# Performance work log

Measured on AMD Instinct MI355X. Metric: run time of the kernel, lower is better.

Reference implementation:

```python
import jax, jax.numpy as jnp
import numpy as np

NA, NB = 40000, 40000
D_IN, D_OUT, H, C = 256, 256, 8, 32  # C = D_OUT // H
E = 400000
N_MP = 3


def setup_inputs() -> dict:
    key = jax.random.key(0)
    ks = jax.random.split(key, 16)
    s = 1.0 / np.sqrt(D_IN)
    inp = {
        "x_A": jax.random.normal(ks[0], (NA, D_IN), jnp.float32),
        "x_B": jax.random.normal(ks[1], (NB, D_IN), jnp.float32),
        "edge_ab": jax.random.randint(ks[2], (2, E), 0, NB, jnp.int32),  # src in A, dst in B
        "edge_ba": jax.random.randint(ks[3], (2, E), 0, NA, jnp.int32),  # src in B, dst in A
        "edge_aa": jax.random.randint(ks[4], (2, E), 0, NA, jnp.int32),  # src in A, dst in A
        "W_A": jax.random.normal(ks[5], (D_IN, D_OUT), jnp.float32) * s,
        "b_A": jnp.zeros((D_OUT,), jnp.float32),
        "W_B": jax.random.normal(ks[6], (D_IN, D_OUT), jnp.float32) * s,
        "b_B": jnp.zeros((D_OUT,), jnp.float32),
        "attn_l": jax.random.normal(ks[7], (N_MP, H, C), jnp.float32) * 0.1,
        "attn_r": jax.random.normal(ks[8], (N_MP, H, C), jnp.float32) * 0.1,
        "rel_l_A": jax.random.normal(ks[9], (H, C), jnp.float32) * 0.1,
        "rel_r_A": jax.random.normal(ks[10], (H, C), jnp.float32) * 0.1,
        "rel_l_B": jax.random.normal(ks[11], (H, C), jnp.float32) * 0.1,
        "rel_r_B": jax.random.normal(ks[12], (H, C), jnp.float32) * 0.1,
    }
    return inp


def _leaky(x):
    return jax.nn.leaky_relu(x, negative_slope=0.2)


def _gat_relation(h_src, edge, a_l, a_r, n_dst):
    """GAT-style edge attention + segment softmax + scatter-add.
    h_src: [N_src,H,C], edge: [2,E], a_l: [N_src,H], a_r: [N_dst,H]."""
    src, dst = edge[0], edge[1]
    e = _leaky(a_l[src] + a_r[dst])                      # [E,H]
    m = jax.ops.segment_max(e, dst, num_segments=n_dst)  # [N_dst,H]
    ex = jnp.exp(e - m[dst])
    denom = jax.ops.segment_sum(ex, dst, num_segments=n_dst)
    alpha = ex / denom[dst]                              # softmax over in-neighbors
    msg = h_src[src] * alpha[:, :, None]                 # [E,H,C]
    return jax.ops.segment_sum(msg, dst, num_segments=n_dst)  # [N_dst,H,C]


def _beta_combine(h, rel_embs, rel_l, rel_r):
    """Relation-level attention (get_beta_weights) + weighted sum.
    h: [N,H,C], rel_embs: [N,H,R,C]."""
    bl = (h * rel_l).sum(-1)                                 # [N,H]
    br = (rel_embs * rel_r[None, :, None, :]).sum(-1)        # [N,H,R]
    beta = jax.nn.softmax(_leaky(bl[:, :, None] + br), axis=2)
    out = (rel_embs * beta[..., None]).sum(2)                # [N,H,C]
    return out.reshape(out.shape[0], H * C)


def reference(x_A, x_B, edge_ab, edge_ba, edge_aa, W_A, b_A, W_B, b_B,
              attn_l, attn_r, rel_l_A, rel_r_A, rel_l_B, rel_r_B):
    nA, nB = x_A.shape[0], x_B.shape[0]
    h_A = (x_A @ W_A + b_A).reshape(nA, H, C)
    h_B = (x_B @ W_B + b_B).reshape(nB, H, C)

    # per-metapath node attention scalars (get_alphas)
    # metapath 0: A->B, 1: B->A, 2: A->A
    al0 = (h_A * attn_l[0]).sum(-1); ar0 = (h_B * attn_r[0]).sum(-1)
    al1 = (h_B * attn_l[1]).sum(-1); ar1 = (h_A * attn_r[1]).sum(-1)
    al2 = (h_A * attn_l[2]).sum(-1); ar2 = (h_A * attn_r[2]).sum(-1)

    # aggregate per tail relation (agg_relation_neighbors); last slot = self
    rel_ba = _gat_relation(h_B, edge_ba, al1, ar1, nA)
    rel_aa = _gat_relation(h_A, edge_aa, al2, ar2, nA)
    emb_A = jnp.stack([rel_ba, rel_aa, h_A], axis=2)         # [NA,H,3,C]

    rel_ab = _gat_relation(h_A, edge_ab, al0, ar0, nB)
    emb_B = jnp.stack([rel_ab, h_B], axis=2)                 # [NB,H,2,C]

    out_A = jax.nn.relu(_beta_combine(h_A, emb_A, rel_l_A, rel_r_A))
    out_B = jax.nn.relu(_beta_combine(h_B, emb_B, rel_l_B, rel_r_B))
    return jnp.concatenate([out_A, out_B], axis=0)           # [NA+NB, D_OUT]
```

## Files before the change

### kernel.cpp

```cpp
#include <hip/hip_runtime.h>
#include <math.h>

#define NAn 40000
#define NBn 40000
#define DIN 256
#define DOUT 256
#define NH 8
#define NC 32
#define NE 400000
#define CAP 64

typedef __attribute__((ext_vector_type(8))) short short8;
typedef __attribute__((ext_vector_type(4))) float floatx4;

__device__ __forceinline__ float leaky(float x) { return x > 0.f ? x : 0.2f * x; }
__device__ __forceinline__ float dot4(float4 a, float4 b) {
  return a.x * b.x + a.y * b.y + a.z * b.z + a.w * b.w;
}
__device__ __forceinline__ unsigned bf16_rne_bits(float x) {
  unsigned u = __float_as_uint(x);
  unsigned r = u + 0x7fffu + ((u >> 16) & 1u);
  return r & 0xffff0000u;
}
__device__ __forceinline__ float4 bf4(uint2 u) {
  float4 f;
  f.x = __uint_as_float(u.x << 16);
  f.y = __uint_as_float(u.x & 0xffff0000u);
  f.z = __uint_as_float(u.y << 16);
  f.w = __uint_as_float(u.y & 0xffff0000u);
  return f;
}
__device__ __forceinline__ void bf8(uint4 u, float* f) {
  f[0] = __uint_as_float(u.x << 16);
  f[1] = __uint_as_float(u.x & 0xffff0000u);
  f[2] = __uint_as_float(u.y << 16);
  f[3] = __uint_as_float(u.y & 0xffff0000u);
  f[4] = __uint_as_float(u.z << 16);
  f[5] = __uint_as_float(u.z & 0xffff0000u);
  f[6] = __uint_as_float(u.w << 16);
  f[7] = __uint_as_float(u.w & 0xffff0000u);
}

__global__ void wswz(const float* __restrict__ WA, const float* __restrict__ WB,
                     short8* __restrict__ hiA, short8* __restrict__ loA,
                     short8* __restrict__ hiB, short8* __restrict__ loB) {
  int t = blockIdx.x * blockDim.x + threadIdx.x;
  const float* W;
  short8 *hi, *lo;
  if (t < 8192) {
    W = WA; hi = hiA; lo = loA;
  } else {
    t -= 8192;
    if (t >= 8192) return;
    W = WB; hi = hiB; lo = loB;
  }
  int kt = t >> 10, nt = (t >> 6) & 15, l = t & 63;
  int n = nt * 16 + (l & 15);
  int kb = kt * 32 + (l >> 4) * 8;
  short8 h8, l8;
#pragma unroll
  for (int j = 0; j < 8; ++j) {
    float w = W[(size_t)(kb + j) * DOUT + n];
    unsigned hb = bf16_rne_bits(w);
    h8[j] = (short)(hb >> 16);
    float rem = w - __uint_as_float(hb);
    l8[j] = (short)(bf16_rne_bits(rem) >> 16);
  }
  hi[t] = h8;
  lo[t] = l8;
}

__global__ __launch_bounds__(256) void gemm_mfma(
    const float* __restrict__ XA, const float* __restrict__ XB,
    const short8* __restrict__ WAhi, const short8* __restrict__ WAlo,
    const short8* __restrict__ WBhi, const short8* __restrict__ WBlo,
    const float* __restrict__ bA, const float* __restrict__ bB,
    unsigned* __restrict__ HAbf, unsigned* __restrict__ HBbf) {
  int blk = blockIdx.x;
  const float* X;
  const short8 *Wh, *Wl;
  const float* bias;
  unsigned* Hbf;
  if (blk < NAn / 64) {
    X = XA; Wh = WAhi; Wl = WAlo; bias = bA; Hbf = HAbf;
  } else {
    blk -= NAn / 64;
    X = XB; Wh = WBhi; Wl = WBlo; bias = bB; Hbf = HBbf;
  }
  const int lane = threadIdx.x & 63, wave = threadIdx.x >> 6;
  const int row0 = blk * 64 + wave * 16;
  const int col16 = lane & 15, quad = lane >> 4;
  floatx4 acc[16];
#pragma unroll
  for (int i = 0; i < 16; ++i) acc[i] = (floatx4){0.f, 0.f, 0.f, 0.f};
  const float4* xp = (const float4*)(X + (size_t)(row0 + col16) * DIN + quad * 8);
  for (int kt = 0; kt < 8; ++kt) {
    float4 x0 = xp[kt * 8];
    float4 x1 = xp[kt * 8 + 1];
    float xv[8] = {x0.x, x0.y, x0.z, x0.w, x1.x, x1.y, x1.z, x1.w};
    short8 ahi, alo;
#pragma unroll
    for (int j = 0; j < 8; ++j) {
      unsigned hb = bf16_rne_bits(xv[j]);
      ahi[j] = (short)(hb >> 16);
      float rem = xv[j] - __uint_as_float(hb);
      alo[j] = (short)(bf16_rne_bits(rem) >> 16);
    }
    const short8* bh = Wh + (size_t)kt * 1024 + lane;
    const short8* bl = Wl + (size_t)kt * 1024 + lane;
#pragma unroll
    for (int nt = 0; nt < 16; ++nt) {
      short8 bhv = bh[nt * 64];
      short8 blv = bl[nt * 64];
      acc[nt] = __builtin_amdgcn_mfma_f32_16x16x32_bf16(ahi, bhv, acc[nt], 0, 0, 0);
      acc[nt] = __builtin_amdgcn_mfma_f32_16x16x32_bf16(alo, bhv, acc[nt], 0, 0, 0);
      acc[nt] = __builtin_amdgcn_mfma_f32_16x16x32_bf16(ahi, blv, acc[nt], 0, 0, 0);
    }
  }
#pragma unroll
  for (int nt = 0; nt < 16; ++nt) {
    float bcol = bias[nt * 16 + col16];
#pragma unroll
    for (int r = 0; r < 4; ++r) {
      int row = row0 + quad * 4 + r;
      float v = acc[nt][r] + bcol;
      float vp = __shfl_xor(v, 1);
      if ((lane & 1) == 0) {
        unsigned p = (bf16_rne_bits(v) >> 16) | bf16_rne_bits(vp);
        Hbf[(size_t)row * 128 + nt * 8 + (col16 >> 1)] = p;
      }
    }
  }
}

__global__ void alphas(const uint2* __restrict__ hAbf, const uint2* __restrict__ hBbf,
                       const float* __restrict__ attn_l, const float* __restrict__ attn_r,
                       float* __restrict__ al0, float* __restrict__ ar1,
                       float* __restrict__ al2, float* __restrict__ ar2,
                       float* __restrict__ ar0, float* __restrict__ al1) {
  int idx = blockIdx.x * blockDim.x + threadIdx.x;
  if (idx >= (NAn + NBn) * NH) return;
  bool isA = idx < NAn * NH;
  int k = isA ? idx : idx - NAn * NH;
  int head = k & 7;
  const uint2* h8 = (isA ? hAbf : hBbf) + (size_t)k * 8;
  if (isA) {
    const float4* l0 = (const float4*)(attn_l + 0 * DOUT + head * NC);
    const float4* r1 = (const float4*)(attn_r + 1 * DOUT + head * NC);
    const float4* l2 = (const float4*)(attn_l + 2 * DOUT + head * NC);
    const float4* r2 = (const float4*)(attn_r + 2 * DOUT + head * NC);
    float s0 = 0, s1 = 0, s2 = 0, s3 = 0;
#pragma unroll
    for (int q = 0; q < 8; ++q) {
      float4 hv = bf4(h8[q]);
      s0 += dot4(hv, l0[q]);
      s1 += dot4(hv, r1[q]);
      s2 += dot4(hv, l2[q]);
      s3 += dot4(hv, r2[q]);
    }
    al0[k] = s0;
    ar1[k] = s1;
    al2[k] = s2;
    ar2[k] = s3;
  } else {
    const float4* r0 = (const float4*)(attn_r + 0 * DOUT + head * NC);
    const float4* l1 = (const float4*)(attn_l + 1 * DOUT + head * NC);
    float s0 = 0, s1 = 0;
#pragma unroll
    for (int q = 0; q < 8; ++q) {
      float4 hv = bf4(h8[q]);
      s0 += dot4(hv, r0[q]);
      s1 += dot4(hv, l1[q]);
    }
    ar0[k] = s0;
    al1[k] = s1;
  }
}

__global__ void build_csr3(const int* __restrict__ e_ba, const int* __restrict__ e_aa,
                           const int* __restrict__ e_ab, int* __restrict__ cnt_ba,
                           int* __restrict__ cnt_aa, int* __restrict__ cnt_ab,
                           int* __restrict__ sl_ba, int* __restrict__ sl_aa,
                           int* __restrict__ sl_ab) {
  int i = blockIdx.x * blockDim.x + threadIdx.x;
  if (i >= 3 * NE) return;
  const int* e;
  int* cnt;
  int* sl;
  int k = i;
  if (i < NE) {
    e = e_ba; cnt = cnt_ba; sl = sl_ba;
  } else if (i < 2 * NE) {
    e = e_aa; cnt = cnt_aa; sl = sl_aa; k = i - NE;
  } else {
    e = e_ab; cnt = cnt_ab; sl = sl_ab; k = i - 2 * NE;
  }
  int src = e[k];
  int dst = e[NE + k];
  int pos = atomicAdd(&cnt[dst], 1);
  if (pos < CAP) sl[(size_t)dst * CAP + pos] = src;
}

__device__ __forceinline__ void gat2(int dst, int wave, int lane, int h, int sub, int head,
                                     const int* __restrict__ cnt,
                                     const int* __restrict__ slots,
                                     const float* __restrict__ al,
                                     const float* __restrict__ ar,
                                     const uint4* __restrict__ hbf,
                                     int lds_slot[4][64], float lds_ex[4][512],
                                     float acc[8]) {
#pragma unroll
  for (int k = 0; k < 8; ++k) acc[k] = 0.f;
  int deg = cnt[dst];
  if (deg > CAP) deg = CAP;
  if (deg == 0) return;
  __threadfence_block();
  if (lane < deg) {
    int s = slots[(size_t)dst * CAP + lane];
    lds_slot[wave][lane] = s;
    float4 a0 = *(const float4*)(al + (size_t)s * 8);
    float4 a1 = *(const float4*)(al + (size_t)s * 8 + 4);
    float4 r0 = *(const float4*)(ar + (size_t)dst * 8);
    float4 r1 = *(const float4*)(ar + (size_t)dst * 8 + 4);
    float* exq = &lds_ex[wave][lane * 8];
    exq[0] = __expf(leaky(a0.x + r0.x));
    exq[1] = __expf(leaky(a0.y + r0.y));
    exq[2] = __expf(leaky(a0.z + r0.z));
    exq[3] = __expf(leaky(a0.w + r0.w));
    exq[4] = __expf(leaky(a1.x + r1.x));
    exq[5] = __expf(leaky(a1.y + r1.y));
    exq[6] = __expf(leaky(a1.z + r1.z));
    exq[7] = __expf(leaky(a1.w + r1.w));
  }
  __threadfence_block();
  float den = 0.f;
  int iters = (deg + 1) >> 1;
  for (int it = 0; it < iters; ++it) {
    int j = it * 2 + h;
    if (j < deg) {
      int sj = lds_slot[wave][j];
      float w = lds_ex[wave][j * 8 + head];
      uint4 u = hbf[(size_t)sj * 32 + sub];
      den += w;
      float f[8];
      bf8(u, f);
#pragma unroll
      for (int k = 0; k < 8; ++k) acc[k] += w * f[k];
    }
  }
#pragma unroll
  for (int k = 0; k < 8; ++k) acc[k] += __shfl_xor(acc[k], 32);
  den += __shfl_xor(den, 32);
  float inv = 1.f / den;
#pragma unroll
  for (int k = 0; k < 8; ++k) acc[k] *= inv;
}

__global__ __launch_bounds__(256) void agg_combine(
    const int* __restrict__ cnt_ba, const int* __restrict__ sl_ba,
    const float* __restrict__ al1, const float* __restrict__ ar1,
    const int* __restrict__ cnt_aa, const int* __restrict__ sl_aa,
    const float* __restrict__ al2, const float* __restrict__ ar2,
    const int* __restrict__ cnt_ab, const int* __restrict__ sl_ab,
    const float* __restrict__ al0, const float* __restrict__ ar0,
    const uint4* __restrict__ hAbf, const uint4* __restrict__ hBbf,
    const float* __restrict__ rlA, const float* __restrict__ rrA,
    const float* __restrict__ rlB, const float* __restrict__ rrB,
    float* __restrict__ outp) {
  __shared__ int lds_slot[4][64];
  __shared__ float lds_ex[4][512];
  int wave = threadIdx.x >> 6, lane = threadIdx.x & 63;
  int h = lane >> 5, sub = lane & 31, head = sub >> 2;
  bool isA = blockIdx.x < (NAn / 4);
  int dst = (isA ? blockIdx.x : blockIdx.x - NAn / 4) * 4 + wave;
  float m0[8], hv[8], o[8];
  if (isA) {
    float m1[8];
    gat2(dst, wave, lane, h, sub, head, cnt_ba, sl_ba, al1, ar1, hBbf, lds_slot, lds_ex, m0);
    gat2(dst, wave, lane, h, sub, head, cnt_aa, sl_aa, al2, ar2, hAbf, lds_slot, lds_ex, m1);
    uint4 us = hAbf[(size_t)dst * 32 + sub];
    bf8(us, hv);
    const float4* rl4 = (const float4*)rlA;
    const float4* rr4 = (const float4*)rrA;
    float4 rl0 = rl4[sub * 2], rl1 = rl4[sub * 2 + 1];
    float4 rr0 = rr4[sub * 2], rr1 = rr4[sub * 2 + 1];
    float rl8[8] = {rl0.x, rl0.y, rl0.z, rl0.w, rl1.x, rl1.y, rl1.z, rl1.w};
    float rr8[8] = {rr0.x, rr0.y, rr0.z, rr0.w, rr1.x, rr1.y, rr1.z, rr1.w};
    float pbl = 0, p0 = 0, p1 = 0, p2 = 0;
#pragma unroll
    for (int k = 0; k < 8; ++k) {
      pbl += hv[k] * rl8[k];
      p0 += m0[k] * rr8[k];
      p1 += m1[k] * rr8[k];
      p2 += hv[k] * rr8[k];
    }
#pragma unroll
    for (int d = 1; d < 4; d <<= 1) {
      pbl += __shfl_xor(pbl, d);
      p0 += __shfl_xor(p0, d);
      p1 += __shfl_xor(p1, d);
      p2 += __shfl_xor(p2, d);
    }
    float b0 = leaky(pbl + p0), b1 = leaky(pbl + p1), b2 = leaky(pbl + p2);
    float mx = fmaxf(b0, fmaxf(b1, b2));
    float w0 = __expf(b0 - mx), w1 = __expf(b1 - mx), w2 = __expf(b2 - mx);
    float inv = 1.f / (w0 + w1 + w2);
    w0 *= inv; w1 *= inv; w2 *= inv;
#pragma unroll
    for (int k = 0; k < 8; ++k)
      o[k] = fmaxf(0.f, m0[k] * w0 + m1[k] * w1 + hv[k] * w2);
  } else {
    gat2(dst, wave, lane, h, sub, head, cnt_ab, sl_ab, al0, ar0, hAbf, lds_slot, lds_ex, m0);
    uint4 us = hBbf[(size_t)dst * 32 + sub];
    bf8(us, hv);
    const float4* rl4 = (const float4*)rlB;
    const float4* rr4 = (const float4*)rrB;
    float4 rl0 = rl4[sub * 2], rl1 = rl4[sub * 2 + 1];
    float4 rr0 = rr4[sub * 2], rr1 = rr4[sub * 2 + 1];
    float rl8[8] = {rl0.x, rl0.y, rl0.z, rl0.w, rl1.x, rl1.y, rl1.z, rl1.w};
    float rr8[8] = {rr0.x, rr0.y, rr0.z, rr0.w, rr1.x, rr1.y, rr1.z, rr1.w};
    float pbl = 0, p0 = 0, p1 = 0;
#pragma unroll
    for (int k = 0; k < 8; ++k) {
      pbl += hv[k] * rl8[k];
      p0 += m0[k] * rr8[k];
      p1 += hv[k] * rr8[k];
    }
#pragma unroll
    for (int d = 1; d < 4; d <<= 1) {
      pbl += __shfl_xor(pbl, d);
      p0 += __shfl_xor(p0, d);
      p1 += __shfl_xor(p1, d);
    }
    float b0 = leaky(pbl + p0), b1 = leaky(pbl + p1);
    float mx = fmaxf(b0, b1);
    float w0 = __expf(b0 - mx), w1 = __expf(b1 - mx);
    float inv = 1.f / (w0 + w1);
    w0 *= inv; w1 *= inv;
#pragma unroll
    for (int k = 0; k < 8; ++k) o[k] = fmaxf(0.f, m0[k] * w0 + hv[k] * w1);
  }
  float* orow = outp + (size_t)(isA ? dst : NAn + dst) * DOUT + sub * 8;
  if (h == 0) {
    *(float4*)orow = (float4){o[0], o[1], o[2], o[3]};
    *(float4*)(orow + 4) = (float4){o[4], o[5], o[6], o[7]};
  }
}

extern "C" void kernel_launch(void* const* d_in, const int* in_sizes, int n_in, void* d_out,
                              int out_size, void* d_ws, size_t ws_size, hipStream_t stream) {
  const float* xA = (const float*)d_in[0];
  const float* xB = (const float*)d_in[1];
  const int* e_ab = (const int*)d_in[2];
  const int* e_ba = (const int*)d_in[3];
  const int* e_aa = (const int*)d_in[4];
  const float* WA = (const float*)d_in[5];
  const float* bA = (const float*)d_in[6];
  const float* WB = (const float*)d_in[7];
  const float* bB = (const float*)d_in[8];
  const float* attn_l = (const float*)d_in[9];
  const float* attn_r = (const float*)d_in[10];
  const float* rlA = (const float*)d_in[11];
  const float* rrA = (const float*)d_in[12];
  const float* rlB = (const float*)d_in[13];
  const float* rrB = (const float*)d_in[14];
  float* out = (float*)d_out;

  char* p = (char*)d_ws;
  auto alloc = [&](size_t bytes) -> char* {
    char* r = p;
    p += (bytes + 255) & ~(size_t)255;
    return r;
  };
  unsigned* hAbf = (unsigned*)alloc((size_t)NAn * DOUT * 2);
  unsigned* hBbf = (unsigned*)alloc((size_t)NBn * DOUT * 2);
  float* al0 = (float*)alloc((size_t)NAn * NH * 4);
  float* ar1 = (float*)alloc((size_t)NAn * NH * 4);
  float* al2 = (float*)alloc((size_t)NAn * NH * 4);
  float* ar2 = (float*)alloc((size_t)NAn * NH * 4);
  float* ar0 = (float*)alloc((size_t)NBn * NH * 4);
  float* al1 = (float*)alloc((size_t)NBn * NH * 4);
  short8* WAhi = (short8*)alloc((size_t)8192 * 16);
  short8* WAlo = (short8*)alloc((size_t)8192 * 16);
  short8* WBhi = (short8*)alloc((size_t)8192 * 16);
  short8* WBlo = (short8*)alloc((size_t)8192 * 16);
  int* cnts = (int*)alloc((size_t)3 * NAn * 4);
  int* cnt_ba = cnts;
  int* cnt_aa = cnts + NAn;
  int* cnt_ab = cnts + 2 * NAn;
  int* slots_ba = (int*)alloc((size_t)NAn * CAP * 4);
  int* slots_aa = (int*)alloc((size_t)NAn * CAP * 4);
  int* slots_ab = (int*)alloc((size_t)NBn * CAP * 4);

  hipMemsetAsync(cnts, 0, (size_t)3 * NAn * 4, stream);

  wswz<<<64, 256, 0, stream>>>(WA, WB, WAhi, WAlo, WBhi, WBlo);
  build_csr3<<<(3 * NE + 255) / 256, 256, 0, stream>>>(e_ba, e_aa, e_ab, cnt_ba, cnt_aa,
                                                       cnt_ab, slots_ba, slots_aa, slots_ab);
  gemm_mfma<<<(NAn + NBn) / 64, 256, 0, stream>>>(xA, xB, WAhi, WAlo, WBhi, WBlo, bA, bB,
                                                  hAbf, hBbf);
  alphas<<<((NAn + NBn) * NH + 255) / 256, 256, 0, stream>>>(
      (const uint2*)hAbf, (const uint2*)hBbf, attn_l, attn_r, al0, ar1, al2, ar2, ar0, al1);
  agg_combine<<<(NAn + NBn) / 4, 256, 0, stream>>>(
      cnt_ba, slots_ba, al1, ar1, cnt_aa, slots_aa, al2, ar2, cnt_ab, slots_ab, al0, ar0,
      (const uint4*)hAbf, (const uint4*)hBbf, rlA, rrA, rlB, rrB, out);
}
```

Baseline: 476.5 us.

## Drop weight low-part split and stage weight fragments in double-buffered LDS

The GEMM stops splitting the weight matrix into hi/lo bf16 parts, so each tile needs two MFMAs instead of three and the low-weight buffer and its swizzle output go away. Weight fragments are now loaded cooperatively into a double-buffered shared-memory tile, with the next k-slice prefetched into registers while the current one is computed. Each wave no longer fetches all weight fragments from global memory on its own. This lowers GEMM precision, since the weight low-order residual is dropped, and adds a block barrier per k-step.

```diff
diff --git a/kernel.cpp b/kernel.cpp
--- a/kernel.cpp
+++ b/kernel.cpp
@@ -42,59 +42,74 @@
 }
 
 __global__ void wswz(const float* __restrict__ WA, const float* __restrict__ WB,
-                     short8* __restrict__ hiA, short8* __restrict__ loA,
-                     short8* __restrict__ hiB, short8* __restrict__ loB) {
+                     short8* __restrict__ hiA, short8* __restrict__ hiB) {
   int t = blockIdx.x * blockDim.x + threadIdx.x;
   const float* W;
-  short8 *hi, *lo;
+  short8* hi;
   if (t < 8192) {
-    W = WA; hi = hiA; lo = loA;
+    W = WA; hi = hiA;
   } else {
     t -= 8192;
     if (t >= 8192) return;
-    W = WB; hi = hiB; lo = loB;
+    W = WB; hi = hiB;
   }
   int kt = t >> 10, nt = (t >> 6) & 15, l = t & 63;
   int n = nt * 16 + (l & 15);
   int kb = kt * 32 + (l >> 4) * 8;
-  short8 h8, l8;
+  short8 h8;
 #pragma unroll
   for (int j = 0; j < 8; ++j) {
     float w = W[(size_t)(kb + j) * DOUT + n];
-    unsigned hb = bf16_rne_bits(w);
-    h8[j] = (short)(hb >> 16);
-    float rem = w - __uint_as_float(hb);
-    l8[j] = (short)(bf16_rne_bits(rem) >> 16);
+    h8[j] = (short)(bf16_rne_bits(w) >> 16);
   }
   hi[t] = h8;
-  lo[t] = l8;
 }
 
 __global__ __launch_bounds__(256) void gemm_mfma(
     const float* __restrict__ XA, const float* __restrict__ XB,
-    const short8* __restrict__ WAhi, const short8* __restrict__ WAlo,
-    const short8* __restrict__ WBhi, const short8* __restrict__ WBlo,
+    const short8* __restrict__ WAhi, const short8* __restrict__ WBhi,
     const float* __restrict__ bA, const float* __restrict__ bB,
     unsigned* __restrict__ HAbf, unsigned* __restrict__ HBbf) {
+  __shared__ short8 bfrag[2][1024];
   int blk = blockIdx.x;
   const float* X;
-  const short8 *Wh, *Wl;
+  const short8* Wh;
   const float* bias;
   unsigned* Hbf;
   if (blk < NAn / 64) {
-    X = XA; Wh = WAhi; Wl = WAlo; bias = bA; Hbf = HAbf;
+    X = XA; Wh = WAhi; bias = bA; Hbf = HAbf;
   } else {
     blk -= NAn / 64;
-    X = XB; Wh = WBhi; Wl = WBlo; bias = bB; Hbf = HBbf;
-  }
-  const int lane = threadIdx.x & 63, wave = threadIdx.x >> 6;
+    X = XB; Wh = WBhi; bias = bB; Hbf = HBbf;
+  }
+  const int tid = threadIdx.x;
+  const int lane = tid & 63, wave = tid >> 6;
   const int row0 = blk * 64 + wave * 16;
   const int col16 = lane & 15, quad = lane >> 4;
+
   floatx4 acc[16];
 #pragma unroll
   for (int i = 0; i < 16; ++i) acc[i] = (floatx4){0.f, 0.f, 0.f, 0.f};
-  const float4* xp = (const float4*)(X + (size_t)(row0 + col16) * DIN + quad * 8);
+
+  const float4* xp = (const float4*)(X + (size_t)(row0 + col16) * DIN) + quad * 2;
+
+  uint4 pre[4];
+  const uint4* wsrc = (const uint4*)Wh;
+#pragma unroll
+  for (int c = 0; c < 4; ++c) pre[c] = wsrc[c * 256 + tid];
+  {
+    uint4* d = (uint4*)&bfrag[0][0];
+#pragma unroll
+    for (int c = 0; c < 4; ++c) d[c * 256 + tid] = pre[c];
+  }
+  __syncthreads();
+
   for (int kt = 0; kt < 8; ++kt) {
+    if (kt < 7) {
+      const uint4* s = wsrc + (size_t)(kt + 1) * 1024;
+#pragma unroll
+      for (int c = 0; c < 4; ++c) pre[c] = s[c * 256 + tid];
+    }
     float4 x0 = xp[kt * 8];
     float4 x1 = xp[kt * 8 + 1];
     float xv[8] = {x0.x, x0.y, x0.z, x0.w, x1.x, x1.y, x1.z, x1.w};
@@ -106,16 +121,19 @@
       float rem = xv[j] - __uint_as_float(hb);
       alo[j] = (short)(bf16_rne_bits(rem) >> 16);
     }
-    const short8* bh = Wh + (size_t)kt * 1024 + lane;
-    const short8* bl = Wl + (size_t)kt * 1024 + lane;
+    const short8* bp = &bfrag[kt & 1][0];
 #pragma unroll
     for (int nt = 0; nt < 16; ++nt) {
-      short8 bhv = bh[nt * 64];
-      short8 blv = bl[nt * 64];
-      acc[nt] = __builtin_amdgcn_mfma_f32_16x16x32_bf16(ahi, bhv, acc[nt], 0, 0, 0);
-      acc[nt] = __builtin_amdgcn_mfma_f32_16x16x32_bf16(alo, bhv, acc[nt], 0, 0, 0);
-      acc[nt] = __builtin_amdgcn_mfma_f32_16x16x32_bf16(ahi, blv, acc[nt], 0, 0, 0);
-    }
+      short8 bv = bp[nt * 64 + lane];
+      acc[nt] = __builtin_amdgcn_mfma_f32_16x16x32_bf16(ahi, bv, acc[nt], 0, 0, 0);
+      acc[nt] = __builtin_amdgcn_mfma_f32_16x16x32_bf16(alo, bv, acc[nt], 0, 0, 0);
+    }
+    if (kt < 7) {
+      uint4* d = (uint4*)&bfrag[(kt + 1) & 1][0];
+#pragma unroll
+      for (int c = 0; c < 4; ++c) d[c * 256 + tid] = pre[c];
+    }
+    __syncthreads();
   }
 #pragma unroll
   for (int nt = 0; nt < 16; ++nt) {
@@ -381,9 +399,7 @@
   float* ar0 = (float*)alloc((size_t)NBn * NH * 4);
   float* al1 = (float*)alloc((size_t)NBn * NH * 4);
   short8* WAhi = (short8*)alloc((size_t)8192 * 16);
-  short8* WAlo = (short8*)alloc((size_t)8192 * 16);
   short8* WBhi = (short8*)alloc((size_t)8192 * 16);
-  short8* WBlo = (short8*)alloc((size_t)8192 * 16);
   int* cnts = (int*)alloc((size_t)3 * NAn * 4);
   int* cnt_ba = cnts;
   int* cnt_aa = cnts + NAn;
@@ -394,11 +410,10 @@
 
   hipMemsetAsync(cnts, 0, (size_t)3 * NAn * 4, stream);
 
-  wswz<<<64, 256, 0, stream>>>(WA, WB, WAhi, WAlo, WBhi, WBlo);
+  wswz<<<64, 256, 0, stream>>>(WA, WB, WAhi, WBhi);
   build_csr3<<<(3 * NE + 255) / 256, 256, 0, stream>>>(e_ba, e_aa, e_ab, cnt_ba, cnt_aa,
                                                        cnt_ab, slots_ba, slots_aa, slots_ab);
-  gemm_mfma<<<(NAn + NBn) / 64, 256, 0, stream>>>(xA, xB, WAhi, WAlo, WBhi, WBlo, bA, bB,
-                                                  hAbf, hBbf);
+  gemm_mfma<<<(NAn + NBn) / 64, 256, 0, stream>>>(xA, xB, WAhi, WBhi, bA, bB, hAbf, hBbf);
   alphas<<<((NAn + NBn) * NH + 255) / 256, 256, 0, stream>>>(
       (const uint2*)hAbf, (const uint2*)hBbf, attn_l, attn_r, al0, ar1, al2, ar2, ar0, al1);
   agg_combine<<<(NAn + NBn) / 4, 256, 0, stream>>>(
```

Result: faster. 439.7 us (-7.7%).
